# Kernel optimization log

Measured on AMD Instinct MI355X. Metric: run time of the kernel, lower is better.

The kernel has to match this reference:

```python
import jax, jax.numpy as jnp
import numpy as np

MAX_ITER = 10
EPS = 1e-4


def setup_inputs() -> dict:
    key = jax.random.key(0)
    k1, k2, k3 = jax.random.split(key, 3)
    B, N, M = 64, 1024, 1024
    s = jax.random.uniform(k1, (B, N, M), dtype=jnp.float32)
    nrows = jax.random.randint(k2, (B,), 0, N, dtype=jnp.int64 if jax.config.read('jax_enable_x64') else jnp.int32)
    ncols = jax.random.randint(k3, (B,), 0, M, dtype=nrows.dtype)
    return {"s": s, "nrows": nrows, "ncols": ncols}


def _sinkhorn(s, nrows, ncols):
    # Faithful to torch Sinkhorn.forward with exp=False, dummy_row=False.
    # The torch code builds [B,N,N]/[B,M,M] block-of-ones matrices and matmuls;
    # mathematically this is a masked column-sum (even iters) / row-sum (odd iters)
    # over the valid nrows[b] x ncols[b] block, followed by division inside the
    # block and zeroing outside it.
    B, N, M = s.shape
    row_mask = jnp.arange(N)[None, :] < nrows[:, None]            # [B, N]
    col_mask = jnp.arange(M)[None, :] < ncols[:, None]            # [B, M]
    mask = row_mask[:, :, None] & col_mask[:, None, :]            # [B, N, M]

    out = s + EPS
    for i in range(MAX_ITER):
        if i % 2 == 0:
            # column sums over valid rows -> [B, 1, M]
            sm = jnp.sum(jnp.where(row_mask[:, :, None], out, 0.0), axis=1, keepdims=True)
        else:
            # row sums over valid cols -> [B, N, 1]
            sm = jnp.sum(jnp.where(col_mask[:, None, :], out, 0.0), axis=2, keepdims=True)
        sm = jnp.where(sm == 0, 1.0, sm)  # guard (only affects masked-out entries)
        out = jnp.where(mask, out / sm, 0.0)
    return out


def reference(s, nrows, ncols):
    return _sinkhorn(s, nrows, ncols)
```

## Files before the change

### kernel.cpp

```cpp
#include <hip/hip_runtime.h>

#define EPS 1e-4f
constexpr int N_DIM = 1024;
constexpr int M_DIM = 1024;

template <bool FIRST>
__global__ void sinkhorn_colupd(const float* __restrict__ s,
                                const int* __restrict__ nrows,
                                const int* __restrict__ ncols,
                                const float* __restrict__ r,
                                float* __restrict__ c) {
    const int b = blockIdx.y;
    const int R = nrows[b];
    const int C = ncols[b];
    const int m0 = blockIdx.x * 64;
    if (m0 >= C) return;

    const int col = threadIdx.x & 63;
    const int rg  = threadIdx.x >> 6;
    const int m   = m0 + col;

    const float* __restrict__ sb = s + (size_t)b * N_DIM * M_DIM;
    const float* __restrict__ rb = r + b * N_DIM;

    float sum = 0.f;
#pragma unroll 4
    for (int n = rg; n < R; n += 4) {
        float v = sb[(size_t)n * M_DIM + m] + EPS;
        sum += FIRST ? v : rb[n] * v;
    }

    __shared__ float red[4][64];
    red[rg][col] = sum;
    __syncthreads();
    if (rg == 0 && m < C) {
        float t = red[0][col] + red[1][col] + red[2][col] + red[3][col];
        c[b * M_DIM + m] = (t == 0.f) ? 1.f : 1.f / t;
    }
}

__global__ void sinkhorn_rowupd(const float* __restrict__ s,
                                const int* __restrict__ nrows,
                                const int* __restrict__ ncols,
                                const float* __restrict__ c,
                                float* __restrict__ r) {
    const int b = blockIdx.y;
    const int R = nrows[b];
    const int C = ncols[b];
    const int n = blockIdx.x * 4 + (threadIdx.x >> 6);
    if (n >= R) return;
    const int lane = threadIdx.x & 63;

    const float* __restrict__ srow = s + ((size_t)b * N_DIM + n) * M_DIM;
    const float* __restrict__ cb   = c + b * M_DIM;

    float sum = 0.f;
    const int C4 = C >> 2;
    const float4* __restrict__ s4 = (const float4*)srow;
    const float4* __restrict__ c4 = (const float4*)cb;
    for (int i = lane; i < C4; i += 64) {
        float4 v = s4[i];
        float4 cc = c4[i];
        sum += (v.x + EPS) * cc.x + (v.y + EPS) * cc.y +
               (v.z + EPS) * cc.z + (v.w + EPS) * cc.w;
    }
    for (int m = C4 * 4 + lane; m < C; m += 64)
        sum += (srow[m] + EPS) * cb[m];

#pragma unroll
    for (int off = 32; off; off >>= 1) sum += __shfl_down(sum, off);
    if (lane == 0)
        r[b * N_DIM + n] = (sum == 0.f) ? 1.f : 1.f / sum;
}

__global__ void sinkhorn_finalize(const float* __restrict__ s,
                                  const int* __restrict__ nrows,
                                  const int* __restrict__ ncols,
                                  const float* __restrict__ r,
                                  const float* __restrict__ c,
                                  float* __restrict__ out) {
    const int n = blockIdx.x;
    const int b = blockIdx.y;
    const int R = nrows[b];
    const int C = ncols[b];
    const size_t base = ((size_t)b * N_DIM + n) * M_DIM;
    const int m = threadIdx.x * 4;

    float4 o = make_float4(0.f, 0.f, 0.f, 0.f);
    if (n < R && m < C) {
        const float rn = r[b * N_DIM + n];
        float4 v  = *(const float4*)(s + base + m);
        float4 cc = *(const float4*)(c + b * M_DIM + m);
        o.x = (m + 0 < C) ? (v.x + EPS) * rn * cc.x : 0.f;
        o.y = (m + 1 < C) ? (v.y + EPS) * rn * cc.y : 0.f;
        o.z = (m + 2 < C) ? (v.z + EPS) * rn * cc.z : 0.f;
        o.w = (m + 3 < C) ? (v.w + EPS) * rn * cc.w : 0.f;
    }
    *(float4*)(out + base + m) = o;
}

extern "C" void kernel_launch(void* const* d_in, const int* in_sizes, int n_in,
                              void* d_out, int out_size, void* d_ws, size_t ws_size,
                              hipStream_t stream) {
    const float* s     = (const float*)d_in[0];
    const int*   nrows = (const int*)d_in[1];
    const int*   ncols = (const int*)d_in[2];
    float*       out   = (float*)d_out;
    const int B = in_sizes[1];

    float* r = (float*)d_ws;
    float* c = r + (size_t)B * N_DIM;

    dim3 colGrid(M_DIM / 64, B);
    dim3 rowGrid(N_DIM / 4, B);

    sinkhorn_colupd<true><<<colGrid, 256, 0, stream>>>(s, nrows, ncols, r, c);
    sinkhorn_rowupd<<<rowGrid, 256, 0, stream>>>(s, nrows, ncols, c, r);
    for (int it = 0; it < 4; ++it) {
        sinkhorn_colupd<false><<<colGrid, 256, 0, stream>>>(s, nrows, ncols, r, c);
        sinkhorn_rowupd<<<rowGrid, 256, 0, stream>>>(s, nrows, ncols, c, r);
    }

    sinkhorn_finalize<<<dim3(N_DIM, B), 256, 0, stream>>>(s, nrows, ncols, r, c, out);
}
```

Baseline: 251.8 us.

## Restructure Sinkhorn sweeps with float4 column tiles, row-chunk partials and LDS-cached scales

The column sweep now reads float4 per lane over 256-column tiles and splits rows into chunks that write partial column sums. The following row sweep reduces those partials and inverts them. Row scaling factors are cached in LDS as reciprocals, and column scales are staged in LDS for row dot products. The aim is wider memory transactions and enough parallelism on the column pass without extra reduction kernels. In exchange, partials are re-reduced redundantly in every row block, and a fallback path exists for a small workspace.

```diff
diff --git a/kernel.cpp b/kernel.cpp
--- a/kernel.cpp
+++ b/kernel.cpp
@@ -3,92 +3,137 @@
 #define EPS 1e-4f
 constexpr int N_DIM = 1024;
 constexpr int M_DIM = 1024;
+constexpr int BATCH = 64;
 
-template <bool FIRST>
-__global__ void sinkhorn_colupd(const float* __restrict__ s,
-                                const int* __restrict__ nrows,
-                                const int* __restrict__ ncols,
-                                const float* __restrict__ r,
-                                float* __restrict__ c) {
-    const int b = blockIdx.y;
-    const int R = nrows[b];
-    const int C = ncols[b];
-    const int m0 = blockIdx.x * 64;
-    if (m0 >= C) return;
 
-    const int col = threadIdx.x & 63;
-    const int rg  = threadIdx.x >> 6;
-    const int m   = m0 + col;
+template <bool FIRST, int CHUNKS>
+__global__ __launch_bounds__(256)
+void col_sweep(const float* __restrict__ s,
+               const int* __restrict__ nrows,
+               const int* __restrict__ ncols,
+               const float* __restrict__ u,
+               float* __restrict__ tpart) {
+    const int b  = blockIdx.y;
+    const int mt = blockIdx.x & 3;
+    const int ch = blockIdx.x >> 2;
+    const int R = nrows[b], C = ncols[b];
+    const int lane = threadIdx.x & 63, wv = threadIdx.x >> 6;
+    const int m0 = mt * 256;
+    const int m  = m0 + lane * 4;
 
-    const float* __restrict__ sb = s + (size_t)b * N_DIM * M_DIM;
-    const float* __restrict__ rb = r + b * N_DIM;
+    constexpr int ROWS = N_DIM / CHUNKS;
+    const int n0 = ch * ROWS;
+    const int nend = min(R, n0 + ROWS);
 
-    float sum = 0.f;
-#pragma unroll 4
-    for (int n = rg; n < R; n += 4) {
-        float v = sb[(size_t)n * M_DIM + m] + EPS;
-        sum += FIRST ? v : rb[n] * v;
+    __shared__ float rlds[1024];
+    if (!FIRST) {
+        for (int i = threadIdx.x; i < ROWS; i += 256) {
+            float uu = u[b * N_DIM + n0 + i];
+            rlds[i] = (uu == 0.f) ? 1.f : 1.f / uu;
+        }
+        __syncthreads();
     }
 
-    __shared__ float red[4][64];
-    red[rg][col] = sum;
+    float4 acc = make_float4(0.f, 0.f, 0.f, 0.f);
+    if (m0 < C) {
+        const float* __restrict__ sb = s + (size_t)b * N_DIM * M_DIM;
+#pragma unroll 4
+        for (int n = n0 + wv; n < nend; n += 4) {
+            float4 v = *(const float4*)(sb + (size_t)n * M_DIM + m);
+            float rn = FIRST ? 1.f : rlds[n - n0];
+            acc.x += rn * (v.x + EPS);
+            acc.y += rn * (v.y + EPS);
+            acc.z += rn * (v.z + EPS);
+            acc.w += rn * (v.w + EPS);
+        }
+    }
+
+    __shared__ float4 red[4][64];
+    red[wv][lane] = acc;
     __syncthreads();
-    if (rg == 0 && m < C) {
-        float t = red[0][col] + red[1][col] + red[2][col] + red[3][col];
-        c[b * M_DIM + m] = (t == 0.f) ? 1.f : 1.f / t;
+    if (wv == 0) {
+        float4 a0 = red[0][lane], a1 = red[1][lane],
+               a2 = red[2][lane], a3 = red[3][lane];
+        float4 t = make_float4(a0.x + a1.x + a2.x + a3.x,
+                               a0.y + a1.y + a2.y + a3.y,
+                               a0.z + a1.z + a2.z + a3.z,
+                               a0.w + a1.w + a2.w + a3.w);
+        *(float4*)(tpart + ((size_t)(ch * BATCH + b)) * M_DIM + m) = t;
     }
 }
 
-__global__ void sinkhorn_rowupd(const float* __restrict__ s,
-                                const int* __restrict__ nrows,
-                                const int* __restrict__ ncols,
-                                const float* __restrict__ c,
-                                float* __restrict__ r) {
+template <int CHUNKS, bool WRITE_C>
+__global__ __launch_bounds__(256)
+void row_sweep(const float* __restrict__ s,
+               const int* __restrict__ nrows,
+               const int* __restrict__ ncols,
+               const float* __restrict__ tpart,
+               float* __restrict__ u,
+               float* __restrict__ cOut) {
     const int b = blockIdx.y;
-    const int R = nrows[b];
-    const int C = ncols[b];
-    const int n = blockIdx.x * 4 + (threadIdx.x >> 6);
-    if (n >= R) return;
-    const int lane = threadIdx.x & 63;
+    const int R = nrows[b], C = ncols[b];
+    const int n0 = blockIdx.x * 16;
+    if (n0 >= R) return;
 
-    const float* __restrict__ srow = s + ((size_t)b * N_DIM + n) * M_DIM;
-    const float* __restrict__ cb   = c + b * M_DIM;
+    __shared__ float clds[M_DIM];
+    {
+        const int t4 = threadIdx.x;
+        float4 sum = make_float4(0.f, 0.f, 0.f, 0.f);
+#pragma unroll
+        for (int ch = 0; ch < CHUNKS; ++ch) {
+            float4 p = *(const float4*)(tpart + ((size_t)(ch * BATCH + b)) * M_DIM + t4 * 4);
+            sum.x += p.x; sum.y += p.y; sum.z += p.z; sum.w += p.w;
+        }
+        float4 cv;
+        cv.x = (sum.x == 0.f) ? 1.f : 1.f / sum.x;
+        cv.y = (sum.y == 0.f) ? 1.f : 1.f / sum.y;
+        cv.z = (sum.z == 0.f) ? 1.f : 1.f / sum.z;
+        cv.w = (sum.w == 0.f) ? 1.f : 1.f / sum.w;
+        *(float4*)&clds[t4 * 4] = cv;
+        if (WRITE_C && blockIdx.x == 0)
+            *(float4*)(cOut + b * M_DIM + t4 * 4) = cv;
+    }
+    __syncthreads();
 
-    float sum = 0.f;
+    const int lane = threadIdx.x & 63, wv = threadIdx.x >> 6;
     const int C4 = C >> 2;
-    const float4* __restrict__ s4 = (const float4*)srow;
-    const float4* __restrict__ c4 = (const float4*)cb;
-    for (int i = lane; i < C4; i += 64) {
-        float4 v = s4[i];
-        float4 cc = c4[i];
-        sum += (v.x + EPS) * cc.x + (v.y + EPS) * cc.y +
-               (v.z + EPS) * cc.z + (v.w + EPS) * cc.w;
+#pragma unroll
+    for (int i = 0; i < 4; ++i) {
+        const int n = n0 + wv * 4 + i;
+        if (n >= R) break;
+        const float* __restrict__ srow = s + ((size_t)b * N_DIM + n) * M_DIM;
+        float sum = 0.f;
+        for (int j = lane; j < C4; j += 64) {
+            float4 v  = ((const float4*)srow)[j];
+            float4 cc = *(const float4*)&clds[j * 4];
+            sum += (v.x + EPS) * cc.x + (v.y + EPS) * cc.y +
+                   (v.z + EPS) * cc.z + (v.w + EPS) * cc.w;
+        }
+        for (int mm = (C4 << 2) + lane; mm < C; mm += 64)
+            sum += (srow[mm] + EPS) * clds[mm];
+#pragma unroll
+        for (int off = 32; off; off >>= 1) sum += __shfl_down(sum, off);
+        if (lane == 0) u[b * N_DIM + n] = sum;
     }
-    for (int m = C4 * 4 + lane; m < C; m += 64)
-        sum += (srow[m] + EPS) * cb[m];
-
-#pragma unroll
-    for (int off = 32; off; off >>= 1) sum += __shfl_down(sum, off);
-    if (lane == 0)
-        r[b * N_DIM + n] = (sum == 0.f) ? 1.f : 1.f / sum;
 }
 
-__global__ void sinkhorn_finalize(const float* __restrict__ s,
-                                  const int* __restrict__ nrows,
-                                  const int* __restrict__ ncols,
-                                  const float* __restrict__ r,
-                                  const float* __restrict__ c,
-                                  float* __restrict__ out) {
+__global__ __launch_bounds__(256)
+void finalize(const float* __restrict__ s,
+              const int* __restrict__ nrows,
+              const int* __restrict__ ncols,
+              const float* __restrict__ u,
+              const float* __restrict__ c,
+              float* __restrict__ out) {
     const int n = blockIdx.x;
     const int b = blockIdx.y;
-    const int R = nrows[b];
-    const int C = ncols[b];
+    const int R = nrows[b], C = ncols[b];
     const size_t base = ((size_t)b * N_DIM + n) * M_DIM;
     const int m = threadIdx.x * 4;
 
     float4 o = make_float4(0.f, 0.f, 0.f, 0.f);
     if (n < R && m < C) {
-        const float rn = r[b * N_DIM + n];
+        float uu = u[b * N_DIM + n];
+        float rn = (uu == 0.f) ? 1.f : 1.f / uu;
         float4 v  = *(const float4*)(s + base + m);
         float4 cc = *(const float4*)(c + b * M_DIM + m);
         o.x = (m + 0 < C) ? (v.x + EPS) * rn * cc.x : 0.f;
@@ -106,20 +151,39 @@
     const int*   nrows = (const int*)d_in[1];
     const int*   ncols = (const int*)d_in[2];
     float*       out   = (float*)d_out;
-    const int B = in_sizes[1];
 
-    float* r = (float*)d_ws;
-    float* c = r + (size_t)B * N_DIM;
+    const size_t needed4 = (size_t)(4 * BATCH * M_DIM + BATCH * N_DIM + BATCH * M_DIM) * 4;
+    const bool big = ws_size >= needed4;
 
-    dim3 colGrid(M_DIM / 64, B);
-    dim3 rowGrid(N_DIM / 4, B);
-
-    sinkhorn_colupd<true><<<colGrid, 256, 0, stream>>>(s, nrows, ncols, r, c);
-    sinkhorn_rowupd<<<rowGrid, 256, 0, stream>>>(s, nrows, ncols, c, r);
-    for (int it = 0; it < 4; ++it) {
-        sinkhorn_colupd<false><<<colGrid, 256, 0, stream>>>(s, nrows, ncols, r, c);
-        sinkhorn_rowupd<<<rowGrid, 256, 0, stream>>>(s, nrows, ncols, c, r);
+    if (big) {
+        constexpr int CH = 4;
+        float* tpart = (float*)d_ws;
+        float* u = tpart + (size_t)CH * BATCH * M_DIM;
+        float* c = u + (size_t)BATCH * N_DIM;
+        dim3 colGrid(4 * CH, BATCH), rowGrid(64, BATCH);
+        col_sweep<true, CH><<<colGrid, 256, 0, stream>>>(s, nrows, ncols, u, tpart);
+        row_sweep<CH, false><<<rowGrid, 256, 0, stream>>>(s, nrows, ncols, tpart, u, c);
+        for (int k = 1; k < 4; ++k) {
+            col_sweep<false, CH><<<colGrid, 256, 0, stream>>>(s, nrows, ncols, u, tpart);
+            row_sweep<CH, false><<<rowGrid, 256, 0, stream>>>(s, nrows, ncols, tpart, u, c);
+        }
+        col_sweep<false, CH><<<colGrid, 256, 0, stream>>>(s, nrows, ncols, u, tpart);
+        row_sweep<CH, true><<<rowGrid, 256, 0, stream>>>(s, nrows, ncols, tpart, u, c);
+        finalize<<<dim3(N_DIM, BATCH), 256, 0, stream>>>(s, nrows, ncols, u, c, out);
+    } else {
+        constexpr int CH = 1;
+        float* tpart = (float*)d_ws;
+        float* u = tpart + (size_t)CH * BATCH * M_DIM;
+        float* c = u + (size_t)BATCH * N_DIM;
+        dim3 colGrid(4 * CH, BATCH), rowGrid(64, BATCH);
+        col_sweep<true, CH><<<colGrid, 256, 0, stream>>>(s, nrows, ncols, u, tpart);
+        row_sweep<CH, false><<<rowGrid, 256, 0, stream>>>(s, nrows, ncols, tpart, u, c);
+        for (int k = 1; k < 4; ++k) {
+            col_sweep<false, CH><<<colGrid, 256, 0, stream>>>(s, nrows, ncols, u, tpart);
+            row_sweep<CH, false><<<rowGrid, 256, 0, stream>>>(s, nrows, ncols, tpart, u, c);
+        }
+        col_sweep<false, CH><<<colGrid, 256, 0, stream>>>(s, nrows, ncols, u, tpart);
+        row_sweep<CH, true><<<rowGrid, 256, 0, stream>>>(s, nrows, ncols, tpart, u, c);
+        finalize<<<dim3(N_DIM, BATCH), 256, 0, stream>>>(s, nrows, ncols, u, c, out);
     }
-
-    sinkhorn_finalize<<<dim3(N_DIM, B), 256, 0, stream>>>(s, nrows, ncols, r, c, out);
 }
```

Result: faster. 244.3 us (-3.0%).
